# Kernel tuning notes

Hardware: AMD Instinct MI355X
Metric: run time of the kernel (lower is better)

Reference implementation:

```python
import jax, jax.numpy as jnp
import numpy as np

NUM_ITERS = 5
NUM_SPATIAL = 3          # S: xyz spatial dims
THETA_ALPHA = 1.0
THETA_BETA = 1.0
THETA_GAMMA = 8.0


def _gauss_filter(f, q):
    """Exact Gaussian filtering (math the permutohedral lattice pl.apply approximates).
    f: [D, N] features, q: [C, N] values.
    out[:, i] = sum_j exp(-0.5 * ||f_i - f_j||^2) * q[:, j]
    """
    f2 = jnp.sum(f * f, axis=0)                       # [N]
    d2 = f2[:, None] + f2[None, :] - 2.0 * (f.T @ f)  # [N, N] squared distances
    K = jnp.exp(-0.5 * d2)                            # symmetric Gaussian kernel
    return q @ K                                      # [C, N]


def setup_inputs() -> dict:
    key = jax.random.key(0)
    k1, k2 = jax.random.split(key)
    C, N, D = 10, 8192, 6
    unaries = jax.random.normal(k1, (C, N), dtype=jnp.float32)
    feat = jax.random.normal(k2, (D, N), dtype=jnp.float32)
    # learned params: diagonal init for filter weights, Potts (-I) compatibility
    spatial_weights = jnp.eye(C, dtype=jnp.float32)
    bilateral_weights = jnp.eye(C, dtype=jnp.float32)
    compatibility_matrix = -jnp.eye(C, dtype=jnp.float32)
    return {
        "unaries": unaries,
        "feat": feat,
        "spatial_weights": spatial_weights,
        "bilateral_weights": bilateral_weights,
        "compatibility_matrix": compatibility_matrix,
    }


def reference(unaries, feat, spatial_weights, bilateral_weights, compatibility_matrix):
    # Pre-scaled features (torch code scales per-iteration, but with
    # theta_alpha=theta_beta=1.0 the in-place aliasing division is a no-op).
    sp_feat = feat[:NUM_SPATIAL] / THETA_GAMMA                      # [S, N]
    bl_feat = jnp.concatenate(
        [feat[:NUM_SPATIAL] / THETA_ALPHA, feat[NUM_SPATIAL:] / THETA_BETA],
        axis=0,
    )                                                               # [S+F, N]

    q = unaries
    for _ in range(NUM_ITERS):
        p = jax.nn.softmax(q, axis=0)                               # over classes
        spatial_out = _gauss_filter(sp_feat, p)                     # [C, N]
        bilateral_out = _gauss_filter(bl_feat, p)                   # [C, N]
        message_passing = spatial_weights @ spatial_out + bilateral_weights @ bilateral_out
        pairwise = compatibility_matrix @ message_passing
        q = unaries - pairwise
    return q
```

## Files before the change

kernel.cpp:

```cpp
#include <hip/hip_runtime.h>
#include <math.h>

#define N 8192
#define C 10
#define NUM_ITERS 5
#define FBLOCK 1024
#define JT 1024
#define NWIN (N / JT)
#define IBLK 32
#define NBLK (N / IBLK)
#define LOG2E 1.44269504088896340736f
#define C3 (LOG2E / 64.0f)
#define PROW (JT + 8)

typedef _Float16 half8 __attribute__((ext_vector_type(8)));
typedef _Float16 half4 __attribute__((ext_vector_type(4)));
typedef float f32x4 __attribute__((ext_vector_type(4)));

#define WS_AJS 0
#define WS_AJB (N * 16)
#define WS_PF0 (N * 32)
#define WS_PF1 (N * 64)

struct FilterSmem {
    half4 ajs_l[JT * 2];
    half4 ajb_l[JT * 2];
    _Float16 p_l[16 * PROW];
};
union FusedSmem {
    FilterSmem f[2];
    float rbuf[16 * 1024];
};

static __device__ __forceinline__ half4 expcvt(f32x4 d) {
    half4 r;
    r[0] = (_Float16)__builtin_amdgcn_exp2f(d[0]);
    r[1] = (_Float16)__builtin_amdgcn_exp2f(d[1]);
    r[2] = (_Float16)__builtin_amdgcn_exp2f(d[2]);
    r[3] = (_Float16)__builtin_amdgcn_exp2f(d[3]);
    return r;
}

static __device__ __forceinline__ void stage_write(
    FilterSmem* fb, int t, int c0, int o0,
    float4 r_s, float4 r_b, float4 r_p0, float4 r_p1) {
    ((float4*)fb->ajs_l)[t] = r_s;
    ((float4*)fb->ajb_l)[t] = r_b;
    float4* pd = (float4*)fb->p_l;
    pd[c0 * (PROW / 8) + o0] = r_p0;
    pd[c0 * (PROW / 8) + 64 + o0] = r_p1;
}

__global__ __launch_bounds__(256) void init_kernel(
    const float* __restrict__ unaries, const float* __restrict__ feat,
    half8* __restrict__ ajs8, half8* __restrict__ ajb8,
    _Float16* __restrict__ pf0, _Float16* __restrict__ pf1) {
    int n = blockIdx.x * 256 + threadIdx.x;
    float f6[6];
#pragma unroll
    for (int d = 0; d < 6; ++d) f6[d] = feat[d * N + n];
    float h3 = 0.5f * (f6[0] * f6[0] + f6[1] * f6[1] + f6[2] * f6[2]);
    float h6v = h3 + 0.5f * (f6[3] * f6[3] + f6[4] * f6[4] + f6[5] * f6[5]);
    half8 a = {};
    a[0] = (_Float16)(f6[0] * C3);
    a[1] = (_Float16)(f6[1] * C3);
    a[2] = (_Float16)(f6[2] * C3);
    a[6] = (_Float16)(-h3 * C3);
    a[7] = (_Float16)1.0f;
    ajs8[n] = a;
    half8 b;
#pragma unroll
    for (int d = 0; d < 6; ++d) b[d] = (_Float16)(f6[d] * LOG2E);
    b[6] = (_Float16)(-h6v * LOG2E);
    b[7] = (_Float16)1.0f;
    ajb8[n] = b;

    float q[C];
#pragma unroll
    for (int c = 0; c < C; ++c) q[c] = unaries[c * N + n];
    float m = q[0];
#pragma unroll
    for (int c = 1; c < C; ++c) m = fmaxf(m, q[c]);
    float e[C], s = 0.0f;
#pragma unroll
    for (int c = 0; c < C; ++c) {
        e[c] = __builtin_amdgcn_exp2f((q[c] - m) * LOG2E);
        s += e[c];
    }
    float inv = 1.0f / s;
#pragma unroll
    for (int c = 0; c < C; ++c) pf0[c * N + n] = (_Float16)(e[c] * inv);
#pragma unroll
    for (int c = C; c < 16; ++c) {
        pf0[c * N + n] = (_Float16)0.0f;
        pf1[c * N + n] = (_Float16)0.0f;
    }
}

__global__ __launch_bounds__(FBLOCK, 4) void fused_kernel(
    const float* __restrict__ unaries, const float* __restrict__ feat,
    const float* __restrict__ SW, const float* __restrict__ BW,
    const float* __restrict__ CM,
    const float4* __restrict__ ajsv, const float4* __restrict__ ajbv,
    const _Float16* __restrict__ pf_in, _Float16* __restrict__ pf_out,
    float* __restrict__ out, int is_last) {
    __shared__ FusedSmem sm;
    int t = threadIdx.x;
    int i0 = blockIdx.x * IBLK;
    int lane = t & 63;
    int w = t >> 6;
    int il = lane & 15;
    int quad = lane >> 4;
    int h = quad & 1;
    bool klo = (quad < 2);
    const half4 hz = {};

    half4 b1s0, b1s1, b1b0, b1b1;
#pragma unroll
    for (int s = 0; s < 2; ++s) {
        int i = i0 + s * 16 + il;
        float g0 = feat[0 * N + i], g1 = feat[1 * N + i], g2 = feat[2 * N + i];
        float g3 = feat[3 * N + i], g4 = feat[4 * N + i], g5 = feat[5 * N + i];
        float h3 = 0.5f * (g0 * g0 + g1 * g1 + g2 * g2);
        float h6v = h3 + 0.5f * (g3 * g3 + g4 * g4 + g5 * g5);
        half4 slo = {(_Float16)g0, (_Float16)g1, (_Float16)g2, (_Float16)0.0f};
        half4 shi = {(_Float16)0.0f, (_Float16)0.0f, (_Float16)1.0f, (_Float16)(-h3 * C3)};
        half4 blo = {(_Float16)g0, (_Float16)g1, (_Float16)g2, (_Float16)g3};
        half4 bhi = {(_Float16)g4, (_Float16)g5, (_Float16)1.0f, (_Float16)(-h6v * LOG2E)};
        half4 vs = klo ? (h ? shi : slo) : hz;
        half4 vb = klo ? (h ? bhi : blo) : hz;
        if (s == 0) { b1s0 = vs; b1b0 = vb; } else { b1s1 = vs; b1b1 = vb; }
    }

    f32x4 as0 = {0.f, 0.f, 0.f, 0.f}, as1 = {0.f, 0.f, 0.f, 0.f};
    f32x4 ab0 = {0.f, 0.f, 0.f, 0.f}, ab1 = {0.f, 0.f, 0.f, 0.f};
    const f32x4 zero = {0.f, 0.f, 0.f, 0.f};

    const float4* ps = (const float4*)pf_in;
    int c0 = t >> 6, o0 = t & 63;

    float4 r_s = ajsv[t];
    float4 r_b = ajbv[t];
    float4 r_p0 = ps[c0 * (N / 8) + o0];
    float4 r_p1 = ps[c0 * (N / 8) + 64 + o0];
    stage_write(&sm.f[0], t, c0, o0, r_s, r_b, r_p0, r_p1);
    r_s = ajsv[JT + t];
    r_b = ajbv[JT + t];
    r_p0 = ps[c0 * (N / 8) + 128 + o0];
    r_p1 = ps[c0 * (N / 8) + 192 + o0];
    __syncthreads();

    for (int win = 0; win < NWIN; ++win) {
        FilterSmem* fb = &sm.f[win & 1];
#pragma unroll
        for (int s = 0; s < 2; ++s) {
            int jb = w * 64 + s * 32;
            int j0 = jb, j1 = jb + 16;
            half4 vs0 = fb->ajs_l[(j0 + il) * 2 + h];
            half4 vb0 = fb->ajb_l[(j0 + il) * 2 + h];
            half4 vs1 = fb->ajs_l[(j1 + il) * 2 + h];
            half4 vb1 = fb->ajb_l[(j1 + il) * 2 + h];
            half4 p2_0 = *(const half4*)&fb->p_l[il * PROW + j0 + quad * 4];
            half4 p2_1 = *(const half4*)&fb->p_l[il * PROW + j1 + quad * 4];
            half4 a1s_0 = klo ? vs0 : hz;
            half4 a1b_0 = klo ? vb0 : hz;
            half4 a1s_1 = klo ? vs1 : hz;
            half4 a1b_1 = klo ? vb1 : hz;

            f32x4 d0 = __builtin_amdgcn_mfma_f32_16x16x16f16(a1s_0, b1s0, zero, 0, 0, 0);
            f32x4 d1 = __builtin_amdgcn_mfma_f32_16x16x16f16(a1s_0, b1s1, zero, 0, 0, 0);
            f32x4 d2 = __builtin_amdgcn_mfma_f32_16x16x16f16(a1b_0, b1b0, zero, 0, 0, 0);
            f32x4 d3 = __builtin_amdgcn_mfma_f32_16x16x16f16(a1b_0, b1b1, zero, 0, 0, 0);
            f32x4 d4 = __builtin_amdgcn_mfma_f32_16x16x16f16(a1s_1, b1s0, zero, 0, 0, 0);
            f32x4 d5 = __builtin_amdgcn_mfma_f32_16x16x16f16(a1s_1, b1s1, zero, 0, 0, 0);
            f32x4 d6 = __builtin_amdgcn_mfma_f32_16x16x16f16(a1b_1, b1b0, zero, 0, 0, 0);
            f32x4 d7 = __builtin_amdgcn_mfma_f32_16x16x16f16(a1b_1, b1b1, zero, 0, 0, 0);

            half4 w0 = expcvt(d0), w1 = expcvt(d1), w2 = expcvt(d2), w3 = expcvt(d3);
            half4 w4 = expcvt(d4), w5 = expcvt(d5), w6 = expcvt(d6), w7 = expcvt(d7);

            as0 = __builtin_amdgcn_mfma_f32_16x16x16f16(w0, p2_0, as0, 0, 0, 0);
            as1 = __builtin_amdgcn_mfma_f32_16x16x16f16(w1, p2_0, as1, 0, 0, 0);
            ab0 = __builtin_amdgcn_mfma_f32_16x16x16f16(w2, p2_0, ab0, 0, 0, 0);
            ab1 = __builtin_amdgcn_mfma_f32_16x16x16f16(w3, p2_0, ab1, 0, 0, 0);
            as0 = __builtin_amdgcn_mfma_f32_16x16x16f16(w4, p2_1, as0, 0, 0, 0);
            as1 = __builtin_amdgcn_mfma_f32_16x16x16f16(w5, p2_1, as1, 0, 0, 0);
            ab0 = __builtin_amdgcn_mfma_f32_16x16x16f16(w6, p2_1, ab0, 0, 0, 0);
            ab1 = __builtin_amdgcn_mfma_f32_16x16x16f16(w7, p2_1, ab1, 0, 0, 0);
        }
        if (win + 1 < NWIN) {
            stage_write(&sm.f[(win + 1) & 1], t, c0, o0, r_s, r_b, r_p0, r_p1);
            if (win + 2 < NWIN) {
                int jb2 = (win + 2) * JT;
                r_s = ajsv[jb2 + t];
                r_b = ajbv[jb2 + t];
                r_p0 = ps[c0 * (N / 8) + (jb2 >> 3) + o0];
                r_p1 = ps[c0 * (N / 8) + (jb2 >> 3) + 64 + o0];
            }
        }
        __syncthreads();
    }

    {
        float* rb = sm.rbuf + w * 1024;
#pragma unroll
        for (int r = 0; r < 4; ++r) {
            rb[r * 64 + lane]       = as0[r];
            rb[256 + r * 64 + lane] = as1[r];
            rb[512 + r * 64 + lane] = ab0[r];
            rb[768 + r * 64 + lane] = ab1[r];
        }
    }
    __syncthreads();
    {
        float tot = 0.f;
#pragma unroll
        for (int w2 = 0; w2 < 16; ++w2) tot += sm.rbuf[w2 * 1024 + t];
        sm.rbuf[t] = tot;
    }
    __syncthreads();

    if (t < IBLK) {
        int i = i0 + t;
        int sub = t >> 4, ql = (t & 15) >> 2, rr = t & 3;
        float sp[C], bl[C];
#pragma unroll
        for (int c = 0; c < C; ++c) {
            int base = sub * 256 + rr * 64 + ql * 16 + c;
            sp[c] = sm.rbuf[base];
            bl[c] = sm.rbuf[base + 512];
        }
        float msg[C];
#pragma unroll
        for (int c = 0; c < C; ++c) {
            float m = 0.f;
#pragma unroll
            for (int k = 0; k < C; ++k)
                m += SW[c * C + k] * sp[k] + BW[c * C + k] * bl[k];
            msg[c] = m;
        }
        float qq[C];
#pragma unroll
        for (int c = 0; c < C; ++c) {
            float pw = 0.f;
#pragma unroll
            for (int k = 0; k < C; ++k) pw += CM[c * C + k] * msg[k];
            qq[c] = unaries[c * N + i] - pw;
        }
        if (is_last) {
#pragma unroll
            for (int c = 0; c < C; ++c) out[c * N + i] = qq[c];
        } else {
            float m = qq[0];
#pragma unroll
            for (int c = 1; c < C; ++c) m = fmaxf(m, qq[c]);
            float e[C], s = 0.0f;
#pragma unroll
            for (int c = 0; c < C; ++c) {
                e[c] = __builtin_amdgcn_exp2f((qq[c] - m) * LOG2E);
                s += e[c];
            }
            float inv = 1.0f / s;
#pragma unroll
            for (int c = 0; c < C; ++c) pf_out[c * N + i] = (_Float16)(e[c] * inv);
        }
    }
}

extern "C" void kernel_launch(void* const* d_in, const int* in_sizes, int n_in,
                              void* d_out, int out_size, void* d_ws, size_t ws_size,
                              hipStream_t stream) {
    const float* unaries = (const float*)d_in[0];
    const float* feat    = (const float*)d_in[1];
    const float* SW      = (const float*)d_in[2];
    const float* BW      = (const float*)d_in[3];
    const float* CM      = (const float*)d_in[4];
    float* out = (float*)d_out;

    char* ws = (char*)d_ws;
    half8* ajs    = (half8*)(ws + WS_AJS);
    half8* ajb    = (half8*)(ws + WS_AJB);
    _Float16* pf0 = (_Float16*)(ws + WS_PF0);
    _Float16* pf1 = (_Float16*)(ws + WS_PF1);

    init_kernel<<<N / 256, 256, 0, stream>>>(unaries, feat, ajs, ajb, pf0, pf1);
    const _Float16* pin = pf0;
    _Float16* pout = pf1;
    for (int it = 1; it <= NUM_ITERS; ++it) {
        fused_kernel<<<NBLK, FBLOCK, 0, stream>>>(
            unaries, feat, SW, BW, CM, (const float4*)ajs, (const float4*)ajb,
            pin, pout, out, it == NUM_ITERS ? 1 : 0);
        const _Float16* tmp = pout;
        pout = (_Float16*)pin;
        pin = tmp;
    }
}
```

Measured before the change: 167.5 us.

## Replace LDS double-buffered staging with per-wave direct global loads and register prefetch

Removes the shared-memory staging of lattice features and probabilities, along with the per-window block barriers. Each wave now owns a contiguous slice of N/16 columns and loads its fragments straight from global memory (L2-resident), prefetching the next step into registers. The exp-to-half conversion also switches to packed cvt_pkrtz. The cost is many small uncoalesced half4 global loads per wave in place of shared LDS reuse, plus round-toward-zero conversion instead of round-to-nearest.

```diff
diff --git a/kernel.cpp b/kernel.cpp
--- a/kernel.cpp
+++ b/kernel.cpp
@@ -5,16 +5,16 @@
 #define C 10
 #define NUM_ITERS 5
 #define FBLOCK 1024
-#define JT 1024
-#define NWIN (N / JT)
 #define IBLK 32
 #define NBLK (N / IBLK)
+#define JW (N / 16)
+#define NS (JW / 32)
 #define LOG2E 1.44269504088896340736f
 #define C3 (LOG2E / 64.0f)
-#define PROW (JT + 8)
 
 typedef _Float16 half8 __attribute__((ext_vector_type(8)));
 typedef _Float16 half4 __attribute__((ext_vector_type(4)));
+typedef _Float16 half2 __attribute__((ext_vector_type(2)));
 typedef float f32x4 __attribute__((ext_vector_type(4)));
 
 #define WS_AJS 0
@@ -22,33 +22,15 @@
 #define WS_PF0 (N * 32)
 #define WS_PF1 (N * 64)
 
-struct FilterSmem {
-    half4 ajs_l[JT * 2];
-    half4 ajb_l[JT * 2];
-    _Float16 p_l[16 * PROW];
-};
-union FusedSmem {
-    FilterSmem f[2];
-    float rbuf[16 * 1024];
-};
-
 static __device__ __forceinline__ half4 expcvt(f32x4 d) {
-    half4 r;
-    r[0] = (_Float16)__builtin_amdgcn_exp2f(d[0]);
-    r[1] = (_Float16)__builtin_amdgcn_exp2f(d[1]);
-    r[2] = (_Float16)__builtin_amdgcn_exp2f(d[2]);
-    r[3] = (_Float16)__builtin_amdgcn_exp2f(d[3]);
+    float e0 = __builtin_amdgcn_exp2f(d[0]);
+    float e1 = __builtin_amdgcn_exp2f(d[1]);
+    float e2 = __builtin_amdgcn_exp2f(d[2]);
+    float e3 = __builtin_amdgcn_exp2f(d[3]);
+    half2 lo = __builtin_bit_cast(half2, __builtin_amdgcn_cvt_pkrtz(e0, e1));
+    half2 hi = __builtin_bit_cast(half2, __builtin_amdgcn_cvt_pkrtz(e2, e3));
+    half4 r = {lo[0], lo[1], hi[0], hi[1]};
     return r;
-}
-
-static __device__ __forceinline__ void stage_write(
-    FilterSmem* fb, int t, int c0, int o0,
-    float4 r_s, float4 r_b, float4 r_p0, float4 r_p1) {
-    ((float4*)fb->ajs_l)[t] = r_s;
-    ((float4*)fb->ajb_l)[t] = r_b;
-    float4* pd = (float4*)fb->p_l;
-    pd[c0 * (PROW / 8) + o0] = r_p0;
-    pd[c0 * (PROW / 8) + 64 + o0] = r_p1;
 }
 
 __global__ __launch_bounds__(256) void init_kernel(
@@ -101,10 +83,10 @@
     const float* __restrict__ unaries, const float* __restrict__ feat,
     const float* __restrict__ SW, const float* __restrict__ BW,
     const float* __restrict__ CM,
-    const float4* __restrict__ ajsv, const float4* __restrict__ ajbv,
+    const half4* __restrict__ ajs_g, const half4* __restrict__ ajb_g,
     const _Float16* __restrict__ pf_in, _Float16* __restrict__ pf_out,
     float* __restrict__ out, int is_last) {
-    __shared__ FusedSmem sm;
+    __shared__ float rbuf[16 * 1024];
     int t = threadIdx.x;
     int i0 = blockIdx.x * IBLK;
     int lane = t & 63;
@@ -136,73 +118,51 @@
     f32x4 ab0 = {0.f, 0.f, 0.f, 0.f}, ab1 = {0.f, 0.f, 0.f, 0.f};
     const f32x4 zero = {0.f, 0.f, 0.f, 0.f};
 
-    const float4* ps = (const float4*)pf_in;
-    int c0 = t >> 6, o0 = t & 63;
-
-    float4 r_s = ajsv[t];
-    float4 r_b = ajbv[t];
-    float4 r_p0 = ps[c0 * (N / 8) + o0];
-    float4 r_p1 = ps[c0 * (N / 8) + 64 + o0];
-    stage_write(&sm.f[0], t, c0, o0, r_s, r_b, r_p0, r_p1);
-    r_s = ajsv[JT + t];
-    r_b = ajbv[JT + t];
-    r_p0 = ps[c0 * (N / 8) + 128 + o0];
-    r_p1 = ps[c0 * (N / 8) + 192 + o0];
-    __syncthreads();
-
-    for (int win = 0; win < NWIN; ++win) {
-        FilterSmem* fb = &sm.f[win & 1];
-#pragma unroll
-        for (int s = 0; s < 2; ++s) {
-            int jb = w * 64 + s * 32;
-            int j0 = jb, j1 = jb + 16;
-            half4 vs0 = fb->ajs_l[(j0 + il) * 2 + h];
-            half4 vb0 = fb->ajb_l[(j0 + il) * 2 + h];
-            half4 vs1 = fb->ajs_l[(j1 + il) * 2 + h];
-            half4 vb1 = fb->ajb_l[(j1 + il) * 2 + h];
-            half4 p2_0 = *(const half4*)&fb->p_l[il * PROW + j0 + quad * 4];
-            half4 p2_1 = *(const half4*)&fb->p_l[il * PROW + j1 + quad * 4];
-            half4 a1s_0 = klo ? vs0 : hz;
-            half4 a1b_0 = klo ? vb0 : hz;
-            half4 a1s_1 = klo ? vs1 : hz;
-            half4 a1b_1 = klo ? vb1 : hz;
-
-            f32x4 d0 = __builtin_amdgcn_mfma_f32_16x16x16f16(a1s_0, b1s0, zero, 0, 0, 0);
-            f32x4 d1 = __builtin_amdgcn_mfma_f32_16x16x16f16(a1s_0, b1s1, zero, 0, 0, 0);
-            f32x4 d2 = __builtin_amdgcn_mfma_f32_16x16x16f16(a1b_0, b1b0, zero, 0, 0, 0);
-            f32x4 d3 = __builtin_amdgcn_mfma_f32_16x16x16f16(a1b_0, b1b1, zero, 0, 0, 0);
-            f32x4 d4 = __builtin_amdgcn_mfma_f32_16x16x16f16(a1s_1, b1s0, zero, 0, 0, 0);
-            f32x4 d5 = __builtin_amdgcn_mfma_f32_16x16x16f16(a1s_1, b1s1, zero, 0, 0, 0);
-            f32x4 d6 = __builtin_amdgcn_mfma_f32_16x16x16f16(a1b_1, b1b0, zero, 0, 0, 0);
-            f32x4 d7 = __builtin_amdgcn_mfma_f32_16x16x16f16(a1b_1, b1b1, zero, 0, 0, 0);
-
-            half4 w0 = expcvt(d0), w1 = expcvt(d1), w2 = expcvt(d2), w3 = expcvt(d3);
-            half4 w4 = expcvt(d4), w5 = expcvt(d5), w6 = expcvt(d6), w7 = expcvt(d7);
-
-            as0 = __builtin_amdgcn_mfma_f32_16x16x16f16(w0, p2_0, as0, 0, 0, 0);
-            as1 = __builtin_amdgcn_mfma_f32_16x16x16f16(w1, p2_0, as1, 0, 0, 0);
-            ab0 = __builtin_amdgcn_mfma_f32_16x16x16f16(w2, p2_0, ab0, 0, 0, 0);
-            ab1 = __builtin_amdgcn_mfma_f32_16x16x16f16(w3, p2_0, ab1, 0, 0, 0);
-            as0 = __builtin_amdgcn_mfma_f32_16x16x16f16(w4, p2_1, as0, 0, 0, 0);
-            as1 = __builtin_amdgcn_mfma_f32_16x16x16f16(w5, p2_1, as1, 0, 0, 0);
-            ab0 = __builtin_amdgcn_mfma_f32_16x16x16f16(w6, p2_1, ab0, 0, 0, 0);
-            ab1 = __builtin_amdgcn_mfma_f32_16x16x16f16(w7, p2_1, ab1, 0, 0, 0);
-        }
-        if (win + 1 < NWIN) {
-            stage_write(&sm.f[(win + 1) & 1], t, c0, o0, r_s, r_b, r_p0, r_p1);
-            if (win + 2 < NWIN) {
-                int jb2 = (win + 2) * JT;
-                r_s = ajsv[jb2 + t];
-                r_b = ajbv[jb2 + t];
-                r_p0 = ps[c0 * (N / 8) + (jb2 >> 3) + o0];
-                r_p1 = ps[c0 * (N / 8) + (jb2 >> 3) + 64 + o0];
-            }
-        }
-        __syncthreads();
+    int wbase = w * JW;
+
+    half4 cvs0 = ajs_g[(wbase + il) * 2 + h];
+    half4 cvb0 = ajb_g[(wbase + il) * 2 + h];
+    half4 cvs1 = ajs_g[(wbase + 16 + il) * 2 + h];
+    half4 cvb1 = ajb_g[(wbase + 16 + il) * 2 + h];
+    half4 cp0 = *(const half4*)&pf_in[il * N + wbase + quad * 4];
+    half4 cp1 = *(const half4*)&pf_in[il * N + wbase + 16 + quad * 4];
+
+    for (int k = 0; k < NS; ++k) {
+        int jn = wbase + ((k + 1) & (NS - 1)) * 32;
+        half4 nvs0 = ajs_g[(jn + il) * 2 + h];
+        half4 nvb0 = ajb_g[(jn + il) * 2 + h];
+        half4 nvs1 = ajs_g[(jn + 16 + il) * 2 + h];
+        half4 nvb1 = ajb_g[(jn + 16 + il) * 2 + h];
+        half4 np0 = *(const half4*)&pf_in[il * N + jn + quad * 4];
+        half4 np1 = *(const half4*)&pf_in[il * N + jn + 16 + quad * 4];
+
+        f32x4 d0 = __builtin_amdgcn_mfma_f32_16x16x16f16(cvs0, b1s0, zero, 0, 0, 0);
+        f32x4 d1 = __builtin_amdgcn_mfma_f32_16x16x16f16(cvs0, b1s1, zero, 0, 0, 0);
+        f32x4 d2 = __builtin_amdgcn_mfma_f32_16x16x16f16(cvb0, b1b0, zero, 0, 0, 0);
+        f32x4 d3 = __builtin_amdgcn_mfma_f32_16x16x16f16(cvb0, b1b1, zero, 0, 0, 0);
+        f32x4 d4 = __builtin_amdgcn_mfma_f32_16x16x16f16(cvs1, b1s0, zero, 0, 0, 0);
+        f32x4 d5 = __builtin_amdgcn_mfma_f32_16x16x16f16(cvs1, b1s1, zero, 0, 0, 0);
+        f32x4 d6 = __builtin_amdgcn_mfma_f32_16x16x16f16(cvb1, b1b0, zero, 0, 0, 0);
+        f32x4 d7 = __builtin_amdgcn_mfma_f32_16x16x16f16(cvb1, b1b1, zero, 0, 0, 0);
+
+        half4 w0 = expcvt(d0), w1 = expcvt(d1), w2 = expcvt(d2), w3 = expcvt(d3);
+        half4 w4 = expcvt(d4), w5 = expcvt(d5), w6 = expcvt(d6), w7 = expcvt(d7);
+
+        as0 = __builtin_amdgcn_mfma_f32_16x16x16f16(w0, cp0, as0, 0, 0, 0);
+        as1 = __builtin_amdgcn_mfma_f32_16x16x16f16(w1, cp0, as1, 0, 0, 0);
+        ab0 = __builtin_amdgcn_mfma_f32_16x16x16f16(w2, cp0, ab0, 0, 0, 0);
+        ab1 = __builtin_amdgcn_mfma_f32_16x16x16f16(w3, cp0, ab1, 0, 0, 0);
+        as0 = __builtin_amdgcn_mfma_f32_16x16x16f16(w4, cp1, as0, 0, 0, 0);
+        as1 = __builtin_amdgcn_mfma_f32_16x16x16f16(w5, cp1, as1, 0, 0, 0);
+        ab0 = __builtin_amdgcn_mfma_f32_16x16x16f16(w6, cp1, ab0, 0, 0, 0);
+        ab1 = __builtin_amdgcn_mfma_f32_16x16x16f16(w7, cp1, ab1, 0, 0, 0);
+
+        cvs0 = nvs0; cvb0 = nvb0; cvs1 = nvs1; cvb1 = nvb1;
+        cp0 = np0; cp1 = np1;
     }
 
     {
-        float* rb = sm.rbuf + w * 1024;
+        float* rb = rbuf + w * 1024;
 #pragma unroll
         for (int r = 0; r < 4; ++r) {
             rb[r * 64 + lane]       = as0[r];
@@ -215,8 +175,8 @@
     {
         float tot = 0.f;
 #pragma unroll
-        for (int w2 = 0; w2 < 16; ++w2) tot += sm.rbuf[w2 * 1024 + t];
-        sm.rbuf[t] = tot;
+        for (int w2 = 0; w2 < 16; ++w2) tot += rbuf[w2 * 1024 + t];
+        rbuf[t] = tot;
     }
     __syncthreads();
 
@@ -227,8 +187,8 @@
 #pragma unroll
         for (int c = 0; c < C; ++c) {
             int base = sub * 256 + rr * 64 + ql * 16 + c;
-            sp[c] = sm.rbuf[base];
-            bl[c] = sm.rbuf[base + 512];
+            sp[c] = rbuf[base];
+            bl[c] = rbuf[base + 512];
         }
         float msg[C];
 #pragma unroll
@@ -288,7 +248,7 @@
     _Float16* pout = pf1;
     for (int it = 1; it <= NUM_ITERS; ++it) {
         fused_kernel<<<NBLK, FBLOCK, 0, stream>>>(
-            unaries, feat, SW, BW, CM, (const float4*)ajs, (const float4*)ajb,
+            unaries, feat, SW, BW, CM, (const half4*)ajs, (const half4*)ajb,
             pin, pout, out, it == NUM_ITERS ? 1 : 0);
         const _Float16* tmp = pout;
         pout = (_Float16*)pin;
```

New measurement: 192.7 us. +15.1%, slower.
